# Optimization experiments

Measured on AMD Instinct MI355X. Metric: run time of the kernel, lower is better.

## Reference

```python
import jax, jax.numpy as jnp
import numpy as np
from jax import lax

B, H, W, K = 32, 384, 384, 16
SENT = H * W          # sentinel label for background / padding
THRESH = 0.75


def setup_inputs() -> dict:
    key = jax.random.key(0)
    ks = jax.random.split(key, 20)
    s = 0.1
    def n(k, shp):
        return jax.random.normal(k, shp, jnp.float32) * s
    return {
        'x1': jax.random.normal(ks[0], (B, 1, H, W), jnp.float32),
        'x2': jax.random.normal(ks[1], (B, 1, H, W), jnp.float32),
        'e1_w': n(ks[2], (16, 1, 4, 4)), 'e1_b': n(ks[3], (16,)),
        'e2_w': n(ks[4], (32, 16, 4, 4)), 'e2_b': n(ks[5], (32,)),
        'e3_w': n(ks[6], (64, 32, 4, 4)), 'e3_b': n(ks[7], (64,)),
        'd3_w': n(ks[8], (64, 32, 4, 4)), 'd3_b': n(ks[9], (32,)),
        'd2_w': n(ks[10], (64, 16, 4, 4)), 'd2_b': n(ks[11], (16,)),
        'd1_w': n(ks[12], (32, 1, 4, 4)), 'd1_b': n(ks[13], (1,)),
        'w1': n(ks[14], (32, 32)), 'b1': n(ks[15], (32,)),
        'w2': n(ks[16], (8, 32)), 'b2': n(ks[17], (8,)),
        'w3': n(ks[18], (1, 8)), 'b3': n(ks[19], (1,)),
    }


def _conv(x, w, b):  # Conv2d(k=4, s=2, p=1), torch OIHW weights
    y = lax.conv_general_dilated(x, w, (2, 2), ((1, 1), (1, 1)),
                                 dimension_numbers=('NCHW', 'OIHW', 'NCHW'))
    return y + b[None, :, None, None]


def _convT(x, w, b):  # ConvTranspose2d(k=4, s=2, p=1), torch (in,out,kh,kw) weights
    wf = jnp.flip(w, (2, 3)).transpose(1, 0, 2, 3)  # -> OIHW
    y = lax.conv_general_dilated(x, wf, (1, 1), ((2, 2), (2, 2)), lhs_dilation=(2, 2),
                                 dimension_numbers=('NCHW', 'OIHW', 'NCHW'))
    return y + b[None, :, None, None]


def _autoencoder(x, e1_w, e1_b, e2_w, e2_b, e3_w, e3_b, d3_w, d3_b, d2_w, d2_b, d1_w, d1_b):
    x1 = jax.nn.relu(_conv(x, e1_w, e1_b))
    x2 = jax.nn.relu(_conv(x1, e2_w, e2_b))
    x3 = jax.nn.relu(_conv(x2, e3_w, e3_b))
    d3 = jax.nn.relu(_convT(x3, d3_w, d3_b))
    d3 = jnp.concatenate([d3, x2], axis=1)
    d2 = jax.nn.relu(_convT(d3, d2_w, d2_b))
    d2 = jnp.concatenate([d2, x1], axis=1)
    return jax.nn.sigmoid(_convT(d2, d1_w, d1_b))


def _extract(heat):
    # 8-connected components via iterative min-label propagation, then
    # centroid -> (radius, angle deg mod 360) around image center, sorted by radius.
    fg = heat > THRESH
    idx = jnp.arange(SENT, dtype=jnp.int32).reshape(H, W)
    l0 = jnp.where(fg, idx, SENT)

    def cond(c):
        return c[1]

    def body(c):
        l, _ = c
        pooled = lax.reduce_window(l, jnp.int32(SENT), lax.min, (3, 3), (1, 1), 'SAME')
        nl = jnp.where(fg, jnp.minimum(l, pooled), SENT)
        return nl, jnp.any(nl != l)

    labels, _ = lax.while_loop(cond, body, (l0, jnp.array(True)))
    flat = labels.ravel()
    u = jnp.unique(flat, size=K + 1, fill_value=SENT)[:K]  # up to K component roots
    valid = u < SENT
    n = valid.sum()
    mask = ((flat[None, :] == u[:, None]) & valid[:, None]).astype(jnp.float32)  # (K, HW)
    cnt = jnp.maximum(mask.sum(1), 1.0)
    cols = (jnp.arange(SENT) % W).astype(jnp.float32)
    rows = (jnp.arange(SENT) // W).astype(jnp.float32)
    cx = mask @ cols / cnt
    cy = mask @ rows / cnt
    dx = cx - (W // 2)
    dy = cy - (H // 2)
    r = jnp.sqrt(dx * dx + dy * dy)
    a = jnp.rad2deg(jnp.arctan2(dy, dx)) % 360.0
    order = jnp.argsort(jnp.where(valid, r, jnp.inf))
    r = jnp.where(valid, r, 0.0)[order]
    a = jnp.where(valid, a, 0.0)[order]
    return r, a, n


def _match(r1, a1, n1, r2, a2, n2):
    # greedy nearest-radius matching of the smaller set against the larger,
    # zero padding up to K pairs; diff = (r1-r2, |sin(radians(a1-a2))|)
    swap = n1 > n2
    rA = jnp.where(swap, r2, r1); aA = jnp.where(swap, a2, a1); nA = jnp.where(swap, n2, n1)
    rB = jnp.where(swap, r1, r2); aB = jnp.where(swap, a1, a2); nB = jnp.where(swap, n1, n2)
    iota = jnp.arange(K)

    def step(used, xs):
        i, rAi, aAi = xs
        vi = i < nA
        d = jnp.where(used | (iota >= nB), jnp.inf, jnp.abs(rB - rAi))
        j = jnp.argmin(d)
        dr = rAi - rB[j]
        da = jnp.abs(jnp.sin(jnp.deg2rad(aAi - aB[j])))
        out = jnp.where(vi, jnp.stack([dr, da]), 0.0)
        used = used.at[j].set(used[j] | vi)
        return used, out

    _, ys = lax.scan(step, jnp.zeros(K, bool), (iota, rA, aA))
    return ys.ravel()  # (2K,) interleaved (dr, da) like torch flatten


def _features(x1, x2, enc):
    h1 = _autoencoder(x1, *enc)[:, 0]  # (B,H,W)
    h2 = _autoencoder(x2, *enc)[:, 0]
    r1, a1, n1 = jax.vmap(_extract)(h1)
    r2, a2, n2 = jax.vmap(_extract)(h2)
    return jax.vmap(_match)(r1, a1, n1, r2, a2, n2)  # (B, 2K)


def reference(x1, x2, e1_w, e1_b, e2_w, e2_b, e3_w, e3_b, d3_w, d3_b, d2_w, d2_b, d1_w, d1_b, w1, b1, w2, b2, w3, b3):
    enc = (e1_w, e1_b, e2_w, e2_b, e3_w, e3_b, d3_w, d3_b, d2_w, d2_b, d1_w, d1_b)
    feats = _features(x1, x2, enc)
    h = jax.nn.relu(feats @ w1.T + b1)
    h = jax.nn.relu(h @ w2.T + b2)
    return (h @ w3.T + b3)[:, 0]
```

## Files before the change

### kernel.cpp

```cpp
#include <hip/hip_runtime.h>
#include <math.h>

#define NIMG 32
#define SENTI 147456
#define CAPR 36864
#define LBG 0x7FFFFFFF

__device__ __forceinline__ int uf_load(int* P, int i) {
  return __hip_atomic_load(&P[i], __ATOMIC_RELAXED, __HIP_MEMORY_SCOPE_AGENT);
}
__device__ int uf_find(int* P, int i) {
  int p = uf_load(P, i);
  while (p != i) {
    int gp = uf_load(P, p);
    if (gp != p) atomicMin(&P[i], gp);
    i = p; p = gp;
  }
  return i;
}
__device__ void uf_union(int* P, int a, int b) {
  while (true) {
    a = uf_find(P, a); b = uf_find(P, b);
    if (a == b) return;
    if (a > b) { int t = a; a = b; b = t; }
    int old = atomicMin(&P[b], a);
    if (old == b) return;
    b = old;
  }
}

__device__ __forceinline__ int l_load(int* lab, int i) {
  return __hip_atomic_load(&lab[i], __ATOMIC_RELAXED, __HIP_MEMORY_SCOPE_WORKGROUP);
}
__device__ int l_find(int* lab, int i) {
  int p = l_load(lab, i);
  while (p != i) { int gp = l_load(lab, p); i = p; p = gp; }
  return i;
}
__device__ void l_union(int* lab, int a, int b) {
  while (true) {
    a = l_find(lab, a); b = l_find(lab, b);
    if (a == b) return;
    if (a > b) { int t = a; a = b; b = t; }
    int old = atomicMin(&lab[b], a);
    if (old == b) return;
    b = old;
  }
}

__global__ __launch_bounds__(256) void k_conv_e1(
    const float* __restrict__ x, const float* __restrict__ w,
    const float* __restrict__ bias, float* __restrict__ out)
{
  int idx = blockIdx.x * 256 + threadIdx.x;
  int ox = idx % 192; int t = idx / 192; int oy = t % 192; int img = t / 192;
  const float* xi = x + (size_t)img * 147456;
  float acc[16];
#pragma unroll
  for (int c = 0; c < 16; c++) acc[c] = bias[c];
#pragma unroll
  for (int ky = 0; ky < 4; ky++) {
    int iy = 2 * oy + ky - 1;
    if (iy < 0 || iy >= 384) continue;
    const float* row = xi + iy * 384;
#pragma unroll
    for (int kx = 0; kx < 4; kx++) {
      int ix = 2 * ox + kx - 1;
      if (ix < 0 || ix >= 384) continue;
      float v = row[ix];
#pragma unroll
      for (int c = 0; c < 16; c++) acc[c] = fmaf(v, w[c * 16 + ky * 4 + kx], acc[c]);
    }
  }
  size_t base = (size_t)img * 589824 + (size_t)oy * 192 + ox;
#pragma unroll
  for (int c = 0; c < 16; c++) out[base + (size_t)c * 36864] = fmaxf(acc[c], 0.f);
}

__global__ __launch_bounds__(256) void k_conv_e2(
    const float* __restrict__ in, const float* __restrict__ w,
    const float* __restrict__ bias, float* __restrict__ out)
{
  int idx = blockIdx.x * 256 + threadIdx.x;
  int p = idx % 48; int t = idx / 48; int oy = t % 96; int img = t / 96;
  const float* xin = in + (size_t)img * 589824;
  float accA[32], accB[32];
#pragma unroll
  for (int c = 0; c < 32; c++) { float bv = bias[c]; accA[c] = bv; accB[c] = bv; }
#pragma unroll 1
  for (int ci = 0; ci < 16; ci++) {
    const float* xc = xin + (size_t)ci * 36864;
#pragma unroll
    for (int ky = 0; ky < 4; ky++) {
      int iy = 2 * oy + ky - 1;
      float xv[6];
      if (iy >= 0 && iy < 192) {
        const float* row = xc + iy * 192;
        int c0 = 4 * p - 1;
#pragma unroll
        for (int u = 0; u < 6; u++) {
          int ix = c0 + u;
          xv[u] = (ix >= 0 && ix < 192) ? row[ix] : 0.f;
        }
      } else {
#pragma unroll
        for (int u = 0; u < 6; u++) xv[u] = 0.f;
      }
#pragma unroll
      for (int co = 0; co < 32; co++) {
        float4 wv = *(const float4*)(w + ((size_t)co * 16 + ci) * 16 + ky * 4);
        accA[co] = fmaf(xv[3], wv.w, fmaf(xv[2], wv.z, fmaf(xv[1], wv.y, fmaf(xv[0], wv.x, accA[co]))));
        accB[co] = fmaf(xv[5], wv.w, fmaf(xv[4], wv.z, fmaf(xv[3], wv.y, fmaf(xv[2], wv.x, accB[co]))));
      }
    }
  }
  size_t base = (size_t)img * 294912 + (size_t)oy * 96 + 2 * p;
#pragma unroll
  for (int co = 0; co < 32; co++) {
    float2 v; v.x = fmaxf(accA[co], 0.f); v.y = fmaxf(accB[co], 0.f);
    *(float2*)(out + base + (size_t)co * 9216) = v;
  }
}

__global__ __launch_bounds__(256) void k_conv_e3(
    const float* __restrict__ in, const float* __restrict__ w,
    const float* __restrict__ bias, float* __restrict__ out)
{
  int idx = blockIdx.x * 256 + threadIdx.x;
  int cog = blockIdx.y;
  int p = idx % 24; int t = idx / 24; int oy = t % 48; int img = t / 48;
  const float* xin = in + (size_t)img * 294912;
  float accA[16], accB[16];
#pragma unroll
  for (int c = 0; c < 16; c++) { float bv = bias[cog * 16 + c]; accA[c] = bv; accB[c] = bv; }
#pragma unroll 1
  for (int ci = 0; ci < 32; ci++) {
    const float* xc = xin + (size_t)ci * 9216;
#pragma unroll
    for (int ky = 0; ky < 4; ky++) {
      int iy = 2 * oy + ky - 1;
      float xv[6];
      if (iy >= 0 && iy < 96) {
        const float* row = xc + iy * 96;
        int c0 = 4 * p - 1;
#pragma unroll
        for (int u = 0; u < 6; u++) {
          int ix = c0 + u;
          xv[u] = (ix >= 0 && ix < 96) ? row[ix] : 0.f;
        }
      } else {
#pragma unroll
        for (int u = 0; u < 6; u++) xv[u] = 0.f;
      }
#pragma unroll
      for (int co = 0; co < 16; co++) {
        float4 wv = *(const float4*)(w + ((size_t)(cog * 16 + co) * 32 + ci) * 16 + ky * 4);
        accA[co] = fmaf(xv[3], wv.w, fmaf(xv[2], wv.z, fmaf(xv[1], wv.y, fmaf(xv[0], wv.x, accA[co]))));
        accB[co] = fmaf(xv[5], wv.w, fmaf(xv[4], wv.z, fmaf(xv[3], wv.y, fmaf(xv[2], wv.x, accB[co]))));
      }
    }
  }
  size_t base = (size_t)img * 147456 + (size_t)(cog * 16) * 2304 + (size_t)oy * 48 + 2 * p;
#pragma unroll
  for (int co = 0; co < 16; co++) {
    float2 v; v.x = fmaxf(accA[co], 0.f); v.y = fmaxf(accB[co], 0.f);
    *(float2*)(out + base + (size_t)co * 2304) = v;
  }
}

__global__ __launch_bounds__(256) void k_convt_d3(
    const float* __restrict__ in, const float* __restrict__ w,
    const float* __restrict__ bias, float* __restrict__ out)
{
  int idx = blockIdx.x * 256 + threadIdx.x;
  int cog = blockIdx.y;
  int pg = idx % 12; int t = idx / 12; int oy = t % 96; int img = t / 96;
  int iy1 = (oy + 1) >> 1; int iy0 = iy1 - 1;
  int ky1 = (oy + 1) - 2 * iy1; int ky0 = ky1 + 2;
  bool v1 = (iy1 < 48), v0 = (iy0 >= 0);
  int c0 = 4 * pg - 1;
  float acc[8][8];
#pragma unroll
  for (int co = 0; co < 8; co++) {
    float bv = bias[cog * 8 + co];
#pragma unroll
    for (int j = 0; j < 8; j++) acc[co][j] = bv;
  }
#pragma unroll 1
  for (int ci = 0; ci < 64; ci++) {
    const float* xc = in + (size_t)img * 147456 + (size_t)ci * 2304;
    const float* r1 = xc + iy1 * 48; const float* r0 = xc + iy0 * 48;
    float x1[6], x0[6];
#pragma unroll
    for (int u = 0; u < 6; u++) {
      int ix = c0 + u;
      bool cb = (ix >= 0) && (ix < 48);
      x1[u] = (v1 && cb) ? r1[ix] : 0.f;
      x0[u] = (v0 && cb) ? r0[ix] : 0.f;
    }
    const float* wb = w + (size_t)ci * 512;
#pragma unroll
    for (int co = 0; co < 8; co++) {
      float4 wv1 = *(const float4*)(wb + (cog * 8 + co) * 16 + ky1 * 4);
      float4 wv0 = *(const float4*)(wb + (cog * 8 + co) * 16 + ky0 * 4);
#pragma unroll
      for (int j = 0; j < 4; j++) {
        acc[co][2 * j]     += x1[j + 1] * wv1.y + x1[j] * wv1.w
                            + x0[j + 1] * wv0.y + x0[j] * wv0.w;
        acc[co][2 * j + 1] += x1[j + 2] * wv1.x + x1[j + 1] * wv1.z
                            + x0[j + 2] * wv0.x + x0[j + 1] * wv0.z;
      }
    }
  }
  size_t base = (size_t)img * 294912 + (size_t)(cog * 8) * 9216 + (size_t)oy * 96 + 8 * pg;
#pragma unroll
  for (int co = 0; co < 8; co++) {
    float4 a, b;
    a.x = fmaxf(acc[co][0], 0.f); a.y = fmaxf(acc[co][1], 0.f);
    a.z = fmaxf(acc[co][2], 0.f); a.w = fmaxf(acc[co][3], 0.f);
    b.x = fmaxf(acc[co][4], 0.f); b.y = fmaxf(acc[co][5], 0.f);
    b.z = fmaxf(acc[co][6], 0.f); b.w = fmaxf(acc[co][7], 0.f);
    *(float4*)(out + base + (size_t)co * 9216)     = a;
    *(float4*)(out + base + (size_t)co * 9216 + 4) = b;
  }
}

__global__ __launch_bounds__(256) void k_convt_d2(
    const float* __restrict__ d3, const float* __restrict__ e2,
    const float* __restrict__ w, const float* __restrict__ bias,
    float* __restrict__ out)
{
  int idx = blockIdx.x * 256 + threadIdx.x;
  int pg = idx % 24; int t = idx / 24; int oy = t % 192; int img = t / 192;
  int iy1 = (oy + 1) >> 1; int iy0 = iy1 - 1;
  int ky1 = (oy + 1) - 2 * iy1; int ky0 = ky1 + 2;
  bool v1 = (iy1 < 96), v0 = (iy0 >= 0);
  int c0 = 4 * pg - 1;
  float acc[16][8];
#pragma unroll
  for (int co = 0; co < 16; co++) {
    float bv = bias[co];
#pragma unroll
    for (int j = 0; j < 8; j++) acc[co][j] = bv;
  }
  for (int half = 0; half < 2; half++) {
    const float* src = (half == 0) ? d3 : e2;
#pragma unroll 1
    for (int ci = 0; ci < 32; ci++) {
      const float* xc = src + (size_t)img * 294912 + (size_t)ci * 9216;
      const float* r1 = xc + iy1 * 96; const float* r0 = xc + iy0 * 96;
      float x1[6], x0[6];
#pragma unroll
      for (int u = 0; u < 6; u++) {
        int ix = c0 + u;
        bool cb = (ix >= 0) && (ix < 96);
        x1[u] = (v1 && cb) ? r1[ix] : 0.f;
        x0[u] = (v0 && cb) ? r0[ix] : 0.f;
      }
      const float* wb = w + (size_t)(half * 32 + ci) * 256;
#pragma unroll
      for (int co = 0; co < 16; co++) {
        float4 wv1 = *(const float4*)(wb + co * 16 + ky1 * 4);
        float4 wv0 = *(const float4*)(wb + co * 16 + ky0 * 4);
#pragma unroll
        for (int j = 0; j < 4; j++) {
          acc[co][2 * j]     += x1[j + 1] * wv1.y + x1[j] * wv1.w
                              + x0[j + 1] * wv0.y + x0[j] * wv0.w;
          acc[co][2 * j + 1] += x1[j + 2] * wv1.x + x1[j + 1] * wv1.z
                              + x0[j + 2] * wv0.x + x0[j + 1] * wv0.z;
        }
      }
    }
  }
  size_t base = (size_t)img * 589824 + (size_t)oy * 192 + 8 * pg;
#pragma unroll
  for (int co = 0; co < 16; co++) {
    float4 a, b;
    a.x = fmaxf(acc[co][0], 0.f); a.y = fmaxf(acc[co][1], 0.f);
    a.z = fmaxf(acc[co][2], 0.f); a.w = fmaxf(acc[co][3], 0.f);
    b.x = fmaxf(acc[co][4], 0.f); b.y = fmaxf(acc[co][5], 0.f);
    b.z = fmaxf(acc[co][6], 0.f); b.w = fmaxf(acc[co][7], 0.f);
    *(float4*)(out + base + (size_t)co * 36864)     = a;
    *(float4*)(out + base + (size_t)co * 36864 + 4) = b;
  }
}

__global__ __launch_bounds__(256) void k_convt_d1(
    const float* __restrict__ d2, const float* __restrict__ e1,
    const float* __restrict__ w, const float* __restrict__ bias,
    int* __restrict__ parent)
{
  int idx = blockIdx.x * 256 + threadIdx.x;
  int p = idx % 192; int t = idx / 192; int oy = t % 384; int img = t / 384;
  int iy1 = (oy + 1) >> 1; int iy0 = iy1 - 1;
  int ky1 = (oy + 1) - 2 * iy1; int ky0 = ky1 + 2;
  bool v1 = (iy1 < 192), v0 = (iy0 >= 0);
  bool pm = (p > 0), pp = (p < 191);
  float zA = bias[0], zB = bias[0];
  for (int half = 0; half < 2; half++) {
    const float* src = (half == 0) ? d2 : e1;
#pragma unroll 1
    for (int ci = 0; ci < 16; ci++) {
      const float* xc = src + (size_t)img * 589824 + (size_t)ci * 36864;
      const float* r1 = xc + iy1 * 192; const float* r0 = xc + iy0 * 192;
      float x1m = (v1 && pm) ? r1[p - 1] : 0.f;
      float x1c = v1 ? r1[p] : 0.f;
      float x1p = (v1 && pp) ? r1[p + 1] : 0.f;
      float x0m = (v0 && pm) ? r0[p - 1] : 0.f;
      float x0c = v0 ? r0[p] : 0.f;
      float x0p = (v0 && pp) ? r0[p + 1] : 0.f;
      const float* wb = w + (size_t)(half * 16 + ci) * 16;
      float4 wv1 = *(const float4*)(wb + ky1 * 4);
      float4 wv0 = *(const float4*)(wb + ky0 * 4);
      zA += x1c * wv1.y + x1m * wv1.w + x0c * wv0.y + x0m * wv0.w;
      zB += x1p * wv1.x + x1c * wv1.z + x0p * wv0.x + x0c * wv0.z;
    }
  }
  const float LN3 = 1.0986122886681098f;
  int* P = parent + (size_t)img * SENTI;
  int pixA = oy * 384 + 2 * p;
  P[pixA]     = (zA > LN3) ? pixA : SENTI;
  P[pixA + 1] = (zB > LN3) ? (pixA + 1) : SENTI;
}

__global__ __launch_bounds__(256) void k_tile_uf(int* __restrict__ parent)
{
  __shared__ int lab[1024];
  int img = blockIdx.y;
  int tile = blockIdx.x;
  int tx = tile % 12, ty = tile / 12;
  int tid = threadIdx.x;
  int* P = parent + (size_t)img * SENTI;
  int gbase = (ty * 32) * 384 + tx * 32;
  bool fg[4];
#pragma unroll
  for (int s = 0; s < 4; s++) {
    int c = tid + s * 256;
    int ly = c >> 5, lx = c & 31;
    int v = P[gbase + ly * 384 + lx];
    fg[s] = (v < SENTI);
    lab[c] = fg[s] ? c : LBG;
  }
  __syncthreads();
#pragma unroll
  for (int s = 0; s < 4; s++) {
    int c = tid + s * 256;
    if (!fg[s]) continue;
    int ly = c >> 5, lx = c & 31;
    if (lx > 0              && l_load(lab, c - 1)  != LBG) l_union(lab, c, c - 1);
    if (ly > 0) {
      if (                     l_load(lab, c - 32) != LBG) l_union(lab, c, c - 32);
      if (lx > 0            && l_load(lab, c - 33) != LBG) l_union(lab, c, c - 33);
      if (lx < 31           && l_load(lab, c - 31) != LBG) l_union(lab, c, c - 31);
    }
  }
  __syncthreads();
#pragma unroll
  for (int s = 0; s < 4; s++) {
    int c = tid + s * 256;
    if (!fg[s]) continue;
    int rc = c, q = lab[rc];
    while (q != rc) { rc = q; q = lab[rc]; }
    int rly = rc >> 5, rlx = rc & 31;
    int ly = c >> 5, lx = c & 31;
    P[gbase + ly * 384 + lx] = gbase + rly * 384 + rlx;
  }
}

__global__ __launch_bounds__(256) void k_border(int* __restrict__ parent)
{
  int idx = blockIdx.x * 256 + threadIdx.x;
  int img = idx / SENTI; int p = idx - img * SENTI;
  int* P = parent + (size_t)img * SENTI;
  int x = p % 384; int y = p / 384;
  bool bx = ((x & 31) == 0) && x > 0;
  bool by = ((y & 31) == 0) && y > 0;
  if (!bx && !by) return;
  if (P[p] >= SENTI) return;
  if (bx) {
    if (            P[p - 1]   < SENTI) uf_union(P, p, p - 1);
    if (y > 0   &&  P[p - 385] < SENTI) uf_union(P, p, p - 385);
    if (y < 383 &&  P[p + 383] < SENTI) uf_union(P, p, p + 383);
  }
  if (by) {
    if (            P[p - 384] < SENTI) uf_union(P, p, p - 384);
    if (x > 0   &&  P[p - 385] < SENTI) uf_union(P, p, p - 385);
    if (x < 383 &&  P[p - 383] < SENTI) uf_union(P, p, p - 383);
  }
}

__global__ __launch_bounds__(256) void k_flatten(
    int* __restrict__ parent, int* __restrict__ rootCnt,
    int* __restrict__ rootList, int base)
{
  __shared__ int lcnt;
  __shared__ int lbase;
  __shared__ int llist[256];
  int tid = threadIdx.x;
  if (tid == 0) lcnt = 0;
  __syncthreads();
  int idx = blockIdx.x * 256 + tid;
  int img = idx / SENTI; int p = idx - img * SENTI;
  int* P = parent + (size_t)img * SENTI;
  int v = P[p];
  if (v < SENTI) {
    int r = v, q = P[r];
    while (q != r) { r = q; q = P[r]; }
    P[p] = r;
    if (r == p) {
      int s = atomicAdd(&lcnt, 1);
      llist[s] = p;
    }
  }
  __syncthreads();
  int n = lcnt;
  if (n > 0) {
    if (tid == 0) lbase = atomicAdd(&rootCnt[base + img], n);
    __syncthreads();
    if (tid < n) rootList[(size_t)img * CAPR + lbase + tid] = llist[tid];
  }
}

__global__ __launch_bounds__(256) void k_select(
    const int* __restrict__ rootCnt, const int* __restrict__ rootList,
    int* __restrict__ U, int* __restrict__ NC, int base)
{
  int img = blockIdx.x; int tid = threadIdx.x;
  __shared__ int sv[256];
  int m = rootCnt[base + img]; if (m > CAPR) m = CAPR;
  const int* rl = rootList + (size_t)img * CAPR;
  int prev = -1;
  for (int k = 0; k < 16; k++) {
    int best = SENTI;
    for (int i = tid; i < m; i += 256) {
      int v = rl[i];
      if (v > prev && v < best) best = v;
    }
    sv[tid] = best; __syncthreads();
    for (int s = 128; s > 0; s >>= 1) {
      if (tid < s) sv[tid] = min(sv[tid], sv[tid + s]);
      __syncthreads();
    }
    int sel = sv[0];
    if (tid == 0) U[(base + img) * 16 + k] = sel;
    prev = (sel < SENTI) ? sel : 0x7FFF0000;
    __syncthreads();
  }
  if (tid == 0) NC[base + img] = (m < 16) ? m : 16;
}

__global__ __launch_bounds__(256) void k_stats(
    const int* __restrict__ parent, const int* __restrict__ U,
    int* __restrict__ CNT, float* __restrict__ SX, float* __restrict__ SY, int base)
{
  __shared__ int lc[16]; __shared__ float lx[16], ly[16];
  int tid = threadIdx.x;
  if (tid < 16) { lc[tid] = 0; lx[tid] = 0.f; ly[tid] = 0.f; }
  __syncthreads();
  int img = blockIdx.y; int g = base + img;
  int p = blockIdx.x * 256 + tid;
  int lbl = parent[(size_t)img * SENTI + p];
  if (lbl < SENTI) {
    const int* u = U + g * 16;
    int slot = -1;
#pragma unroll
    for (int s = 0; s < 16; s++) if (u[s] == lbl) slot = s;
    if (slot >= 0) {
      atomicAdd(&lc[slot], 1);
      atomicAdd(&lx[slot], (float)(p % 384));
      atomicAdd(&ly[slot], (float)(p / 384));
    }
  }
  __syncthreads();
  if (tid < 16 && lc[tid] > 0) {
    atomicAdd(&CNT[g * 16 + tid], lc[tid]);
    atomicAdd(&SX[g * 16 + tid], lx[tid]);
    atomicAdd(&SY[g * 16 + tid], ly[tid]);
  }
}

__global__ __launch_bounds__(64) void k_final(
    const int* __restrict__ U, const int* __restrict__ NC,
    const int* __restrict__ CNT, const float* __restrict__ SX,
    const float* __restrict__ SY,
    const float* __restrict__ w1, const float* __restrict__ b1,
    const float* __restrict__ w2, const float* __restrict__ b2,
    const float* __restrict__ w3, const float* __restrict__ b3,
    float* __restrict__ out)
{
  int b = threadIdx.x;
  if (b >= 32) return;
  const float INF = __builtin_inff();
  float R[2][16], A[2][16]; int N[2];
  for (int side = 0; side < 2; side++) {
    int img = b + side * 32;
    float rr[16], aa[16], key[16];
    for (int s = 0; s < 16; s++) {
      bool valid = U[img * 16 + s] < SENTI;
      float c = fmaxf((float)CNT[img * 16 + s], 1.f);
      float cx = SX[img * 16 + s] / c, cy = SY[img * 16 + s] / c;
      float dx = cx - 192.f, dy = cy - 192.f;
      rr[s] = sqrtf(dx * dx + dy * dy);
      float ang = atan2f(dy, dx) * 57.29577951308232f;
      ang = fmodf(ang, 360.f);
      if (ang < 0.f) ang += 360.f;
      aa[s] = ang;
      key[s] = valid ? rr[s] : INF;
    }
    bool taken[16];
    for (int s = 0; s < 16; s++) taken[s] = false;
    for (int k = 0; k < 16; k++) {
      int bi = -1; float bk = 0.f;
      for (int s = 0; s < 16; s++) {
        if (taken[s]) continue;
        if (bi < 0 || key[s] < bk) { bi = s; bk = key[s]; }
      }
      taken[bi] = true;
      bool val = (key[bi] < INF);
      R[side][k] = val ? rr[bi] : 0.f;
      A[side][k] = val ? aa[bi] : 0.f;
    }
    N[side] = NC[img];
  }
  int n1 = N[0], n2 = N[1];
  bool sw = n1 > n2;
  float* rA = sw ? R[1] : R[0];
  float* aA = sw ? A[1] : A[0];
  float* rB = sw ? R[0] : R[1];
  float* aB = sw ? A[0] : A[1];
  int nA = sw ? n2 : n1;
  int nB = sw ? n1 : n2;
  bool used[16];
  for (int s = 0; s < 16; s++) used[s] = false;
  float f[32];
  for (int i = 0; i < 16; i++) {
    bool vi = i < nA;
    float best = 0.f; int j = 0; bool found = false;
    for (int jj = 0; jj < 16; jj++) {
      if (used[jj] || jj >= nB) continue;
      float d = fabsf(rB[jj] - rA[i]);
      if (!found || d < best) { best = d; j = jj; found = true; }
    }
    float dr = rA[i] - rB[j];
    float da = fabsf(sinf((aA[i] - aB[j]) * 0.017453292519943295f));
    f[2 * i]     = vi ? dr : 0.f;
    f[2 * i + 1] = vi ? da : 0.f;
    if (vi) used[j] = true;
  }
  float h1[32];
  for (int jj = 0; jj < 32; jj++) {
    float s = b1[jj];
    for (int k2 = 0; k2 < 32; k2++) s += w1[jj * 32 + k2] * f[k2];
    h1[jj] = fmaxf(s, 0.f);
  }
  float h2[8];
  for (int jj = 0; jj < 8; jj++) {
    float s = b2[jj];
    for (int k2 = 0; k2 < 32; k2++) s += w2[jj * 32 + k2] * h1[k2];
    h2[jj] = fmaxf(s, 0.f);
  }
  float o = b3[0];
  for (int k2 = 0; k2 < 8; k2++) o += w3[k2] * h2[k2];
  out[b] = o;
}

extern "C" void kernel_launch(void* const* d_in, const int* in_sizes, int n_in,
                              void* d_out, int out_size, void* d_ws, size_t ws_size,
                              hipStream_t stream)
{
  (void)in_sizes; (void)n_in; (void)out_size; (void)ws_size;
  const float* x1  = (const float*)d_in[0];
  const float* x2  = (const float*)d_in[1];
  const float* e1w = (const float*)d_in[2];  const float* e1b = (const float*)d_in[3];
  const float* e2w = (const float*)d_in[4];  const float* e2b = (const float*)d_in[5];
  const float* e3w = (const float*)d_in[6];  const float* e3b = (const float*)d_in[7];
  const float* d3w = (const float*)d_in[8];  const float* d3b = (const float*)d_in[9];
  const float* d2w = (const float*)d_in[10]; const float* d2b = (const float*)d_in[11];
  const float* d1w = (const float*)d_in[12]; const float* d1b = (const float*)d_in[13];
  const float* w1  = (const float*)d_in[14]; const float* b1  = (const float*)d_in[15];
  const float* w2  = (const float*)d_in[16]; const float* b2  = (const float*)d_in[17];
  const float* w3  = (const float*)d_in[18]; const float* b3  = (const float*)d_in[19];

  char* ws = (char*)d_ws;
  float* E1 = (float*)(ws + 0);
  float* E2 = (float*)(ws + 75497472);
  float* E3 = (float*)(ws + 113246208);
  float* D3 = (float*)(ws + 132120576);
  float* D2 = (float*)(ws + 169869312);
  char* small = ws + 245366784;
  int* PARENT = (int*)E3;
  int* ROOTL  = (int*)E2;
  int*   ROOTC = (int*)(small);
  int*   U     = (int*)(small + 256);
  int*   NC    = (int*)(small + 4352);
  int*   CNT   = (int*)(small + 4608);
  float* SX    = (float*)(small + 8704);
  float* SY    = (float*)(small + 12800);

  hipMemsetAsync(ROOTC, 0, 256, stream);
  hipMemsetAsync(CNT, 0, 4096, stream);
  hipMemsetAsync(SX, 0, 4096, stream);
  hipMemsetAsync(SY, 0, 4096, stream);

  for (int pass = 0; pass < 2; pass++) {
    const float* x = (pass == 0) ? x1 : x2;
    int base = pass * 32;
    k_conv_e1<<<4608, 256, 0, stream>>>(x, e1w, e1b, E1);
    k_conv_e2<<<576, 256, 0, stream>>>(E1, e2w, e2b, E2);
    k_conv_e3<<<dim3(144, 4), 256, 0, stream>>>(E2, e3w, e3b, E3);
    k_convt_d3<<<dim3(144, 4), 256, 0, stream>>>(E3, d3w, d3b, D3);
    k_convt_d2<<<576, 256, 0, stream>>>(D3, E2, d2w, d2b, D2);
    k_convt_d1<<<9216, 256, 0, stream>>>(D2, E1, d1w, d1b, PARENT);
    k_tile_uf<<<dim3(144, 32), 256, 0, stream>>>(PARENT);
    k_border<<<18432, 256, 0, stream>>>(PARENT);
    k_flatten<<<18432, 256, 0, stream>>>(PARENT, ROOTC, ROOTL, base);
    k_select<<<32, 256, 0, stream>>>(ROOTC, ROOTL, U, NC, base);
    k_stats<<<dim3(576, 32), 256, 0, stream>>>(PARENT, U, CNT, SX, SY, base);
  }
  k_final<<<1, 64, 0, stream>>>(U, NC, CNT, SX, SY, w1, b1, w2, b2, w3, b3, (float*)d_out);
}
```

Measured before the change: 2.857 ms.

## Batch both input passes into a single 64-image pipeline when workspace allows

When the workspace is large enough, both inputs are processed as one 64-image batch instead of two sequential 32-image passes. The first conv kernel picks its input pointer per image, and the grid sizes and workspace offsets scale with the image count. This halves the number of kernel launches and fills the GPU better on the small-grid stages (e3, d3, select). In exchange it needs twice the workspace and falls back to two passes otherwise. It also relies on the downstream kernels indexing correctly for 64 images.

```diff
diff --git a/kernel.cpp b/kernel.cpp
--- a/kernel.cpp
+++ b/kernel.cpp
@@ -1,7 +1,6 @@
 #include <hip/hip_runtime.h>
 #include <math.h>
 
-#define NIMG 32
 #define SENTI 147456
 #define CAPR 36864
 #define LBG 0x7FFFFFFF
@@ -49,12 +48,14 @@
 }
 
 __global__ __launch_bounds__(256) void k_conv_e1(
-    const float* __restrict__ x, const float* __restrict__ w,
-    const float* __restrict__ bias, float* __restrict__ out)
+    const float* __restrict__ xa, const float* __restrict__ xb,
+    const float* __restrict__ w, const float* __restrict__ bias,
+    float* __restrict__ out)
 {
   int idx = blockIdx.x * 256 + threadIdx.x;
   int ox = idx % 192; int t = idx / 192; int oy = t % 192; int img = t / 192;
-  const float* xi = x + (size_t)img * 147456;
+  const float* xi = (img < 32) ? (xa + (size_t)img * 147456)
+                               : (xb + (size_t)(img - 32) * 147456);
   float acc[16];
 #pragma unroll
   for (int c = 0; c < 16; c++) acc[c] = bias[c];
@@ -568,7 +569,7 @@
                               void* d_out, int out_size, void* d_ws, size_t ws_size,
                               hipStream_t stream)
 {
-  (void)in_sizes; (void)n_in; (void)out_size; (void)ws_size;
+  (void)in_sizes; (void)n_in; (void)out_size;
   const float* x1  = (const float*)d_in[0];
   const float* x2  = (const float*)d_in[1];
   const float* e1w = (const float*)d_in[2];  const float* e1b = (const float*)d_in[3];
@@ -581,13 +582,22 @@
   const float* w2  = (const float*)d_in[16]; const float* b2  = (const float*)d_in[17];
   const float* w3  = (const float*)d_in[18]; const float* b3  = (const float*)d_in[19];
 
+  const size_t NEED64 = 490733568ull + 16384ull;
+  bool single = (ws_size >= NEED64);
+  int NI = single ? 64 : 32;
+  int passes = single ? 1 : 2;
+
   char* ws = (char*)d_ws;
-  float* E1 = (float*)(ws + 0);
-  float* E2 = (float*)(ws + 75497472);
-  float* E3 = (float*)(ws + 113246208);
-  float* D3 = (float*)(ws + 132120576);
-  float* D2 = (float*)(ws + 169869312);
-  char* small = ws + 245366784;
+  size_t szE1 = (size_t)NI * 2359296;
+  size_t szE2 = (size_t)NI * 1179648;
+  size_t szE3 = (size_t)NI * 589824;
+  size_t szD3 = (size_t)NI * 1179648;
+  float* E1 = (float*)(ws);
+  float* E2 = (float*)(ws + szE1);
+  float* E3 = (float*)(ws + szE1 + szE2);
+  float* D3 = (float*)(ws + szE1 + szE2 + szE3);
+  float* D2 = (float*)(ws + szE1 + szE2 + szE3 + szD3);
+  char* small = ws + szE1 + szE2 + szE3 + szD3 + szE1;
   int* PARENT = (int*)E3;
   int* ROOTL  = (int*)E2;
   int*   ROOTC = (int*)(small);
@@ -602,20 +612,21 @@
   hipMemsetAsync(SX, 0, 4096, stream);
   hipMemsetAsync(SY, 0, 4096, stream);
 
-  for (int pass = 0; pass < 2; pass++) {
-    const float* x = (pass == 0) ? x1 : x2;
-    int base = pass * 32;
-    k_conv_e1<<<4608, 256, 0, stream>>>(x, e1w, e1b, E1);
-    k_conv_e2<<<576, 256, 0, stream>>>(E1, e2w, e2b, E2);
-    k_conv_e3<<<dim3(144, 4), 256, 0, stream>>>(E2, e3w, e3b, E3);
-    k_convt_d3<<<dim3(144, 4), 256, 0, stream>>>(E3, d3w, d3b, D3);
-    k_convt_d2<<<576, 256, 0, stream>>>(D3, E2, d2w, d2b, D2);
-    k_convt_d1<<<9216, 256, 0, stream>>>(D2, E1, d1w, d1b, PARENT);
-    k_tile_uf<<<dim3(144, 32), 256, 0, stream>>>(PARENT);
-    k_border<<<18432, 256, 0, stream>>>(PARENT);
-    k_flatten<<<18432, 256, 0, stream>>>(PARENT, ROOTC, ROOTL, base);
-    k_select<<<32, 256, 0, stream>>>(ROOTC, ROOTL, U, NC, base);
-    k_stats<<<dim3(576, 32), 256, 0, stream>>>(PARENT, U, CNT, SX, SY, base);
+  for (int pass = 0; pass < passes; pass++) {
+    const float* xa = single ? x1 : ((pass == 0) ? x1 : x2);
+    const float* xb = single ? x2 : xa;
+    int base = single ? 0 : pass * 32;
+    k_conv_e1<<<NI * 144, 256, 0, stream>>>(xa, xb, e1w, e1b, E1);
+    k_conv_e2<<<NI * 18, 256, 0, stream>>>(E1, e2w, e2b, E2);
+    k_conv_e3<<<dim3(NI * 9 / 2, 4), 256, 0, stream>>>(E2, e3w, e3b, E3);
+    k_convt_d3<<<dim3(NI * 9 / 2, 4), 256, 0, stream>>>(E3, d3w, d3b, D3);
+    k_convt_d2<<<NI * 18, 256, 0, stream>>>(D3, E2, d2w, d2b, D2);
+    k_convt_d1<<<NI * 288, 256, 0, stream>>>(D2, E1, d1w, d1b, PARENT);
+    k_tile_uf<<<dim3(144, NI), 256, 0, stream>>>(PARENT);
+    k_border<<<NI * 576, 256, 0, stream>>>(PARENT);
+    k_flatten<<<NI * 576, 256, 0, stream>>>(PARENT, ROOTC, ROOTL, base);
+    k_select<<<NI, 256, 0, stream>>>(ROOTC, ROOTL, U, NC, base);
+    k_stats<<<dim3(576, NI), 256, 0, stream>>>(PARENT, U, CNT, SX, SY, base);
   }
   k_final<<<1, 64, 0, stream>>>(U, NC, CNT, SX, SY, w1, b1, w2, b2, w3, b3, (float*)d_out);
 }
```

Result: slower. 2.970 ms (+3.9%).
